# Kernel optimization log

Measured on AMD Instinct MI355X. Metric: run time of the kernel, lower is better.

## Reference

```python
import jax, jax.numpy as jnp
import numpy as np

N_NODES = 100000
N_EDGES = 1600000
EMBED = 64
HEADS = 8
HEAD_DIM = EMBED // HEADS
FFN = 4 * EMBED
EPS = 1e-5


def _layer_norm(x, g, b):
    m = jnp.mean(x, axis=-1, keepdims=True)
    v = jnp.mean(jnp.square(x - m), axis=-1, keepdims=True)
    return (x - m) * jax.lax.rsqrt(v + EPS) * g + b


def setup_inputs() -> dict:
    key = jax.random.key(0)
    ks = jax.random.split(key, 10)
    s = lambda fan_in: 1.0 / np.sqrt(fan_in)
    x = jax.random.normal(ks[0], (N_NODES, EMBED), dtype=jnp.float32)
    edge_indices = jax.random.randint(ks[1], (2, N_EDGES), 0, N_NODES, dtype=jnp.int64)
    attn_w = jax.random.uniform(ks[2], (EMBED, 3 * EMBED), jnp.float32, -s(EMBED), s(EMBED))
    attn_b = jnp.zeros((3 * EMBED,), jnp.float32)
    w1 = jax.random.uniform(ks[3], (EMBED, FFN), jnp.float32, -s(EMBED), s(EMBED))
    b1 = jnp.zeros((FFN,), jnp.float32)
    w2 = jax.random.uniform(ks[4], (FFN, EMBED), jnp.float32, -s(FFN), s(FFN))
    b2 = jnp.zeros((EMBED,), jnp.float32)
    ln1_g = jnp.ones((EMBED,), jnp.float32)
    ln1_b = jnp.zeros((EMBED,), jnp.float32)
    ln2_g = jnp.ones((EMBED,), jnp.float32)
    ln2_b = jnp.zeros((EMBED,), jnp.float32)
    return {"x": x, "edge_indices": edge_indices, "attn_w": attn_w, "attn_b": attn_b,
            "w1": w1, "b1": b1, "w2": w2, "b2": b2,
            "ln1_g": ln1_g, "ln1_b": ln1_b, "ln2_g": ln2_g, "ln2_b": ln2_b}


def _self_attention(x, edge_indices, attn_w, attn_b):
    n = x.shape[0]
    row, col = edge_indices[0], edge_indices[1]
    scale = EMBED ** (-0.5)  # note: original scales by embed_dim**-0.5
    qkv = (x @ attn_w + attn_b).reshape(n, HEADS, 3 * HEAD_DIM)
    q, k, v = jnp.split(qkv, 3, axis=2)  # each [N, H, Dh]
    alpha = jnp.sum(q[row] * k[col], axis=2) * scale  # [E, H]
    # sparse per-row softmax via segment reductions
    m = jax.ops.segment_max(alpha, row, num_segments=n)  # [N, H]
    e = jnp.exp(alpha - m[row])
    denom = jax.ops.segment_sum(e, row, num_segments=n)  # [N, H]
    weights = e / denom[row]  # [E, H]
    vals = v[col] * weights[:, :, None]  # [E, H, Dh]
    out = jax.ops.segment_sum(vals, row, num_segments=n)  # [N, H, Dh]
    return out.reshape(n, EMBED)


def reference(x, edge_indices, attn_w, attn_b, w1, b1, w2, b2, ln1_g, ln1_b, ln2_g, ln2_b):
    # post-norm (norm_first=False), dropout=0
    x = _layer_norm(x + _self_attention(x, edge_indices, attn_w, attn_b), ln1_g, ln1_b)
    ffn = jax.nn.relu(x @ w1 + b1) @ w2 + b2
    x = _layer_norm(x + ffn, ln2_g, ln2_b)
    return x
```

## Files before the change

### kernel.cpp

```cpp
#include <hip/hip_runtime.h>
#include <hip/hip_bf16.h>


#define WAVE 64
constexpr int BUCKET_SHIFT = 7;
constexpr int NBMAX = 800;

typedef __attribute__((ext_vector_type(8))) short bf16x8;
typedef __attribute__((ext_vector_type(4))) float f32x4;
typedef __attribute__((ext_vector_type(2))) float f32x2;
typedef __attribute__((ext_vector_type(2))) _Float16 h16x2;

__device__ __forceinline__ float bfbits_lo(unsigned u) {
  return __uint_as_float(u << 16);
}
__device__ __forceinline__ float bfbits_hi(unsigned u) {
  return __uint_as_float(u & 0xffff0000u);
}
__device__ __forceinline__ unsigned f2bf_pk(float a, float b) {
  unsigned ua = __float_as_uint(a);
  unsigned ub = __float_as_uint(b);
  ua = (ua + 0x7fff + ((ua >> 16) & 1)) >> 16;
  ub = (ub + 0x7fff + ((ub >> 16) & 1)) & 0xffff0000u;
  return ua | ub;
}
__device__ __forceinline__ unsigned short f2bf1(float a) {
  unsigned ua = __float_as_uint(a);
  ua = (ua + 0x7fff + ((ua >> 16) & 1)) >> 16;
  return (unsigned short)ua;
}

#if defined(__has_builtin)
#if __has_builtin(__builtin_amdgcn_cvt_pkrtz)
#define HAS_PKRTZ 1
#endif
#if __has_builtin(__builtin_amdgcn_fdot2)
#define HAS_FDOT2 1
#endif
#endif

__device__ __forceinline__ unsigned f2h_pk(float a, float b) {
#ifdef HAS_PKRTZ
  auto h = __builtin_amdgcn_cvt_pkrtz(a, b);
  return __builtin_bit_cast(unsigned, h);
#else
  h16x2 h;
  h.x = (_Float16)a;
  h.y = (_Float16)b;
  return __builtin_bit_cast(unsigned, h);
#endif
}

__device__ __forceinline__ float dot8_f16(uint4 kw, uint4 qw) {
#ifdef HAS_FDOT2
  float s = __builtin_amdgcn_fdot2(__builtin_bit_cast(h16x2, kw.x),
                                   __builtin_bit_cast(h16x2, qw.x), 0.f, false);
  s = __builtin_amdgcn_fdot2(__builtin_bit_cast(h16x2, kw.y),
                             __builtin_bit_cast(h16x2, qw.y), s, false);
  s = __builtin_amdgcn_fdot2(__builtin_bit_cast(h16x2, kw.z),
                             __builtin_bit_cast(h16x2, qw.z), s, false);
  s = __builtin_amdgcn_fdot2(__builtin_bit_cast(h16x2, kw.w),
                             __builtin_bit_cast(h16x2, qw.w), s, false);
  return s;
#else
  unsigned kk[4] = {kw.x, kw.y, kw.z, kw.w};
  unsigned qq[4] = {qw.x, qw.y, qw.z, qw.w};
  float s = 0.f;
#pragma unroll
  for (int i = 0; i < 4; i++) {
    h16x2 a = __builtin_bit_cast(h16x2, kk[i]);
    h16x2 b = __builtin_bit_cast(h16x2, qq[i]);
    s += (float)a.x * (float)b.x + (float)a.y * (float)b.y;
  }
  return s;
#endif
}

__device__ __forceinline__ void acc8_f16_pk(uint4 w, h16x2 e2, h16x2 acc[4]) {
  acc[0] = __builtin_elementwise_fma(__builtin_bit_cast(h16x2, w.x), e2, acc[0]);
  acc[1] = __builtin_elementwise_fma(__builtin_bit_cast(h16x2, w.y), e2, acc[1]);
  acc[2] = __builtin_elementwise_fma(__builtin_bit_cast(h16x2, w.z), e2, acc[2]);
  acc[3] = __builtin_elementwise_fma(__builtin_bit_cast(h16x2, w.w), e2, acc[3]);
}

__global__ __launch_bounds__(256) void cvt_w2(
    const float* __restrict__ aw, const float* __restrict__ w1,
    const float* __restrict__ w2, unsigned short* __restrict__ awT,
    unsigned short* __restrict__ w1T, unsigned short* __restrict__ w2T) {
  int tid = blockIdx.x * 256 + threadIdx.x;
  int stride = gridDim.x * 256;
  for (int i = tid; i < 192 * 64; i += stride) {
    int nn = i >> 6, kk = i & 63;
    awT[i] = f2bf1(aw[kk * 192 + nn]);
  }
  for (int i = tid; i < 256 * 64; i += stride) {
    int nn = i >> 6, kk = i & 63;
    w1T[i] = f2bf1(w1[kk * 256 + nn]);
  }
  for (int i = tid; i < 64 * 256; i += stride) {
    int nn = i >> 8, kk = i & 255;
    w2T[i] = f2bf1(w2[kk * 64 + nn]);
  }
}

template <int NCOLS, int K, int MODE>
__global__ __launch_bounds__(256) void mfma_gemm(
    const unsigned short* __restrict__ A, const float* __restrict__ Af,
    const unsigned short* __restrict__ BT, const float* __restrict__ bias,
    unsigned short* __restrict__ out_q, unsigned char* __restrict__ out_kv,
    unsigned short* __restrict__ out_h,
    const unsigned short* __restrict__ resid, const float* __restrict__ g,
    const float* __restrict__ beta, float* __restrict__ out_f, int n) {
  constexpr int KP = K + 8;
  constexpr int NT = NCOLS / 16;
  constexpr int NKC = K / 32;
  __shared__ unsigned short sB[NCOLS * KP];

  const int tid = threadIdx.x;
  {
    const uint4* src = (const uint4*)BT;
    for (int idx = tid; idx < NCOLS * K / 8; idx += 256) {
      int nn = idx / (K / 8), kq = idx % (K / 8);
      *(uint4*)&sB[nn * KP + kq * 8] = src[idx];
    }
  }
  __syncthreads();

  const int wid = tid >> 6, lane = tid & 63;
  const int l15 = lane & 15, quad = lane >> 4;
  const int rowbase = blockIdx.x * 128 + wid * 32;

  bf16x8 afrag[2][NKC];
#pragma unroll
  for (int rg = 0; rg < 2; rg++) {
    int row = rowbase + rg * 16 + l15;
    if (row >= n) row = n - 1;
    if constexpr (MODE == 0) {
      const float4* ap = (const float4*)(Af + (size_t)row * K);
#pragma unroll
      for (int kc = 0; kc < NKC; kc++) {
        float4 a = ap[kc * 8 + quad * 2], b = ap[kc * 8 + quad * 2 + 1];
        union {
          unsigned u[4];
          bf16x8 v;
        } z;
        z.u[0] = f2bf_pk(a.x, a.y);
        z.u[1] = f2bf_pk(a.z, a.w);
        z.u[2] = f2bf_pk(b.x, b.y);
        z.u[3] = f2bf_pk(b.z, b.w);
        afrag[rg][kc] = z.v;
      }
    } else {
      const bf16x8* ap = (const bf16x8*)(A + (size_t)row * K);
#pragma unroll
      for (int kc = 0; kc < NKC; kc++) afrag[rg][kc] = ap[kc * 4 + quad];
    }
  }

  f32x4 acc[2][NT];
#pragma unroll
  for (int rg = 0; rg < 2; rg++)
#pragma unroll
    for (int t = 0; t < NT; t++) acc[rg][t] = (f32x4){0.f, 0.f, 0.f, 0.f};

#pragma unroll
  for (int t = 0; t < NT; t++) {
#pragma unroll
    for (int kc = 0; kc < NKC; kc++) {
      bf16x8 b = *(const bf16x8*)&sB[(t * 16 + l15) * KP + kc * 32 + quad * 8];
      acc[0][t] = __builtin_amdgcn_mfma_f32_16x16x32_bf16(b, afrag[0][kc],
                                                          acc[0][t], 0, 0, 0);
      acc[1][t] = __builtin_amdgcn_mfma_f32_16x16x32_bf16(b, afrag[1][kc],
                                                          acc[1][t], 0, 0, 0);
    }
  }

  if (MODE == 0) {
#pragma unroll
    for (int rg = 0; rg < 2; rg++) {
      int row = rowbase + rg * 16 + l15;
      if (row >= n) continue;
#pragma unroll
      for (int t = 0; t < NT; t++) {
        int c0 = t * 16 + quad * 4;
        float4 bb = *(const float4*)&bias[c0];
        float v0 = acc[rg][t].x + bb.x, v1 = acc[rg][t].y + bb.y;
        float v2 = acc[rg][t].z + bb.z, v3 = acc[rg][t].w + bb.w;
        int hh = c0 / 24, rem = c0 % 24;
        if (rem < 8) {
          v0 *= 0.125f;
          v1 *= 0.125f;
          v2 *= 0.125f;
          v3 *= 0.125f;
          *(uint2*)(out_q + (size_t)row * 64 + hh * 8 + rem) =
              make_uint2(f2h_pk(v0, v1), f2h_pk(v2, v3));
        } else if (rem < 16) {
          *(uint2*)(out_kv + ((size_t)row << 8) + hh * 16 + (rem - 8) * 2) =
              make_uint2(f2h_pk(v0, v1), f2h_pk(v2, v3));
        } else {
          *(uint2*)(out_kv + ((size_t)row << 8) + 128 + hh * 16 +
                    (rem - 16) * 2) =
              make_uint2(f2h_pk(v0, v1), f2h_pk(v2, v3));
        }
      }
    }
  } else if (MODE == 1) {
#pragma unroll
    for (int rg = 0; rg < 2; rg++) {
      int row = rowbase + rg * 16 + l15;
      if (row >= n) continue;
#pragma unroll
      for (int t = 0; t < NT; t++) {
        int c0 = t * 16 + quad * 4;
        float4 bb = *(const float4*)&bias[c0];
        float v0 = fmaxf(acc[rg][t].x + bb.x, 0.f);
        float v1 = fmaxf(acc[rg][t].y + bb.y, 0.f);
        float v2 = fmaxf(acc[rg][t].z + bb.z, 0.f);
        float v3 = fmaxf(acc[rg][t].w + bb.w, 0.f);
        *(uint2*)(out_h + (size_t)row * NCOLS + c0) =
            make_uint2(f2bf_pk(v0, v1), f2bf_pk(v2, v3));
      }
    }
  } else {
#pragma unroll
    for (int rg = 0; rg < 2; rg++) {
      int row = rowbase + rg * 16 + l15;
      bool ok = row < n;
      int rowc = ok ? row : n - 1;
      float vals[4][4];
      float ps = 0.f, pq = 0.f;
#pragma unroll
      for (int t = 0; t < 4; t++) {
        int c0 = t * 16 + quad * 4;
        float4 bb = *(const float4*)&bias[c0];
        uint2 rr = *(const uint2*)&resid[(size_t)rowc * 64 + c0];
        vals[t][0] = acc[rg][t].x + bb.x + bfbits_lo(rr.x);
        vals[t][1] = acc[rg][t].y + bb.y + bfbits_hi(rr.x);
        vals[t][2] = acc[rg][t].z + bb.z + bfbits_lo(rr.y);
        vals[t][3] = acc[rg][t].w + bb.w + bfbits_hi(rr.y);
#pragma unroll
        for (int r = 0; r < 4; r++) {
          ps += vals[t][r];
          pq += vals[t][r] * vals[t][r];
        }
      }
      ps += __shfl_xor(ps, 16);
      ps += __shfl_xor(ps, 32);
      pq += __shfl_xor(pq, 16);
      pq += __shfl_xor(pq, 32);
      float mean = ps * (1.f / 64.f);
      float var = pq * (1.f / 64.f) - mean * mean;
      float inv = rsqrtf(var + 1e-5f);
      if (ok) {
#pragma unroll
        for (int t = 0; t < 4; t++) {
          int c0 = t * 16 + quad * 4;
          float4 gg = *(const float4*)&g[c0];
          float4 be = *(const float4*)&beta[c0];
          float4 o = make_float4((vals[t][0] - mean) * inv * gg.x + be.x,
                                 (vals[t][1] - mean) * inv * gg.y + be.y,
                                 (vals[t][2] - mean) * inv * gg.z + be.z,
                                 (vals[t][3] - mean) * inv * gg.w + be.w);
          *(float4*)&out_f[(size_t)row * 64 + c0] = o;
        }
      }
    }
  }
}

__global__ void detect_kernel(const int* __restrict__ e, unsigned* flag) {
  unsigned v = 0;
  for (int i = threadIdx.x; i < 2048; i += 256) v |= (unsigned)e[2 * i + 1];
#pragma unroll
  for (int m = 1; m < WAVE; m <<= 1) v |= (unsigned)__shfl_xor((int)v, m);
  if ((threadIdx.x & 63) == 0 && v) atomicOr(flag, 1u);
}

__device__ __forceinline__ int edge_row(const int* e, int i, bool is64) {
  return is64 ? e[2 * (size_t)i] : e[i];
}
__device__ __forceinline__ int edge_col(const int* e, int i, int E, bool is64) {
  return is64 ? e[2 * ((size_t)E + i)] : e[(size_t)E + i];
}

__global__ __launch_bounds__(256) void partition_count(
    const int* __restrict__ e, int E, const unsigned* __restrict__ flag,
    int* __restrict__ G, int NB, int CH) {
  __shared__ int h[NBMAX];
  bool is64 = (*flag == 0u);
  for (int b = threadIdx.x; b < NB; b += 256) h[b] = 0;
  __syncthreads();
  int c0 = blockIdx.x * CH, c1 = min(E, c0 + CH);
  for (int i = c0 + threadIdx.x; i < c1; i += 256)
    atomicAdd(&h[edge_row(e, i, is64) >> BUCKET_SHIFT], 1);
  __syncthreads();
  for (int b = threadIdx.x; b < NB; b += 256) G[b * 256 + blockIdx.x] = h[b];
}

__global__ __launch_bounds__(1024) void scan_reduce(const int* __restrict__ in,
                                                    int n,
                                                    int* __restrict__ bsum) {
  __shared__ int sdata[16];
  int tid = threadIdx.x;
  int idx = blockIdx.x * 1024 + tid;
  int v = (idx < n) ? in[idx] : 0;
#pragma unroll
  for (int m = 1; m < WAVE; m <<= 1) v += __shfl_xor(v, m);
  if ((tid & 63) == 0) sdata[tid >> 6] = v;
  __syncthreads();
  if (tid < 16) {
    int s = sdata[tid];
#pragma unroll
    for (int m = 1; m < 16; m <<= 1) s += __shfl_xor(s, m);
    if (tid == 0) bsum[blockIdx.x] = s;
  }
}

__global__ __launch_bounds__(256) void scan_top(const int* __restrict__ bsum,
                                                int nb,
                                                int* __restrict__ bpre) {
  __shared__ int wsum[4];
  int tid = threadIdx.x;
  int lane = tid & 63, wid = tid >> 6;
  int v = (tid < nb) ? bsum[tid] : 0;
  int incl = v;
#pragma unroll
  for (int m = 1; m < WAVE; m <<= 1) {
    int t = __shfl_up(incl, m);
    if (lane >= m) incl += t;
  }
  if (lane == 63) wsum[wid] = incl;
  __syncthreads();
  int add = 0;
  for (int w = 0; w < wid; w++) add += wsum[w];
  if (tid < nb) bpre[tid] = add + incl - v;
}

__global__ __launch_bounds__(1024) void scan_apply(
    const int* __restrict__ in, int n, const int* __restrict__ bpre,
    int* __restrict__ outscan) {
  __shared__ int wtot[16];
  __shared__ int wexcl[16];
  int tid = threadIdx.x;
  int idx = blockIdx.x * 1024 + tid;
  int v = (idx < n) ? in[idx] : 0;
  int incl = v;
#pragma unroll
  for (int m = 1; m < WAVE; m <<= 1) {
    int t = __shfl_up(incl, m);
    if ((tid & 63) >= m) incl += t;
  }
  int wid = tid >> 6;
  if ((tid & 63) == 63) wtot[wid] = incl;
  __syncthreads();
  if (tid < 16) {
    int w = wtot[tid];
    int wi = w;
#pragma unroll
    for (int m = 1; m < 16; m <<= 1) {
      int t = __shfl_up(wi, m);
      if (tid >= m) wi += t;
    }
    wexcl[tid] = wi - w;
  }
  __syncthreads();
  if (idx < n) outscan[idx] = bpre[blockIdx.x] + wexcl[wid] + incl - v;
}

__global__ __launch_bounds__(256) void partition_scatter(
    const int* __restrict__ e, int E, const unsigned* __restrict__ flag,
    const int* __restrict__ scanG, unsigned* __restrict__ ebuf, int NB,
    int CH) {
  __shared__ int base[NBMAX];
  bool is64 = (*flag == 0u);
  for (int b = threadIdx.x; b < NB; b += 256)
    base[b] = scanG[b * 256 + blockIdx.x];
  __syncthreads();
  int c0 = blockIdx.x * CH, c1 = min(E, c0 + CH);
  for (int i = c0 + threadIdx.x; i < c1; i += 256) {
    int r = edge_row(e, i, is64);
    int c = edge_col(e, i, E, is64);
    int pos = atomicAdd(&base[r >> BUCKET_SHIFT], 1);
    ebuf[pos] = ((unsigned)(r & 127) << 17) | (unsigned)c;
  }
}

__global__ __launch_bounds__(256) void bucket_csr(
    const unsigned* __restrict__ ebuf, const int* __restrict__ scanG,
    int* __restrict__ ecol, int* __restrict__ rowstart, int n, int NB, int E) {
  __shared__ int cnt[128], offs[128], cur[128];
  const int b = blockIdx.x;
  const int tid = threadIdx.x;
  const int start = scanG[b * 256];
  const int end = (b + 1 < NB) ? scanG[(b + 1) * 256] : E;
  if (tid < 128) cnt[tid] = 0;
  __syncthreads();
  for (int i = start + tid; i < end; i += 256)
    atomicAdd(&cnt[(ebuf[i] >> 17) & 127], 1);
  __syncthreads();
  if (tid < 128) offs[tid] = cnt[tid];
  __syncthreads();
  for (int s = 1; s < 128; s <<= 1) {
    int t = 0;
    if (tid < 128 && tid >= s) t = offs[tid - s];
    __syncthreads();
    if (tid < 128) offs[tid] += t;
    __syncthreads();
  }
  if (tid < 128) {
    int excl = offs[tid] - cnt[tid];
    cur[tid] = start + excl;
    int gr = (b << BUCKET_SHIFT) + tid;
    if (gr < n) rowstart[gr] = start + excl;
  }
  if (b == NB - 1 && tid == 0) rowstart[n] = E;
  __syncthreads();
  for (int i = start + tid; i < end; i += 256) {
    unsigned p = ebuf[i];
    int pos = atomicAdd(&cur[(p >> 17) & 127], 1);
    ecol[pos] = (int)(p & 0x1FFFF);
  }
}

__global__ __launch_bounds__(256) void attn_ln_kernel(
    const float* __restrict__ x, const unsigned short* __restrict__ qbuf,
    const unsigned char* __restrict__ kv, const int* __restrict__ rowstart,
    const int* __restrict__ ecol, const float* __restrict__ g,
    const float* __restrict__ beta, unsigned short* __restrict__ x1b, int n) {
  int wave = threadIdx.x >> 6;
  int lane = threadIdx.x & 63;
  int node = blockIdx.x * 4 + wave;
  if (node >= n) return;
  const int e = lane >> 3, h = lane & 7;

  uint4 qp = ((const uint4*)qbuf)[(size_t)node * 8 + h];

  int start = rowstart[node];
  int cnt = rowstart[node + 1] - start;
  const int* ec = ecol + start;
  const int koff = h * 16, voff = 128 + h * 16;

  float den = 0.f;
  h16x2 acch[4];
#pragma unroll
  for (int j = 0; j < 4; j++) acch[j] = (h16x2){(_Float16)0.f, (_Float16)0.f};

  int iters = (cnt + 7) >> 3;
  int it = 0;
  for (; it + 2 <= iters; it += 2) {
    int i0 = it * 8 + e;
    int i1 = i0 + 8;
    bool v1 = i1 < cnt;
    int c0 = ec[i0];
    int c1 = ec[v1 ? i1 : i0];
    const unsigned char* r0 = kv + ((size_t)c0 << 8);
    const unsigned char* r1 = kv + ((size_t)c1 << 8);
    uint4 kw0 = *(const uint4*)(r0 + koff);
    uint4 vw0 = *(const uint4*)(r0 + voff);
    uint4 kw1 = *(const uint4*)(r1 + koff);
    uint4 vw1 = *(const uint4*)(r1 + voff);
    float a0 = dot8_f16(kw0, qp);
    float a1 = dot8_f16(kw1, qp);
    float e0 = __expf(a0);
    float e1 = v1 ? __expf(a1) : 0.f;
    den += e0 + e1;
    h16x2 ep0 = __builtin_bit_cast(h16x2, f2h_pk(e0, e0));
    h16x2 ep1 = __builtin_bit_cast(h16x2, f2h_pk(e1, e1));
    acc8_f16_pk(vw0, ep0, acch);
    acc8_f16_pk(vw1, ep1, acch);
  }
  if (it < iters) {
    int i0 = it * 8 + e;
    bool v0 = i0 < cnt;
    int c0 = ec[v0 ? i0 : 0];
    const unsigned char* r0 = kv + ((size_t)c0 << 8);
    uint4 kw0 = *(const uint4*)(r0 + koff);
    uint4 vw0 = *(const uint4*)(r0 + voff);
    float a0 = dot8_f16(kw0, qp);
    float e0 = v0 ? __expf(a0) : 0.f;
    den += e0;
    h16x2 ep0 = __builtin_bit_cast(h16x2, f2h_pk(e0, e0));
    acc8_f16_pk(vw0, ep0, acch);
  }

#pragma unroll
  for (int m = 8; m < 64; m <<= 1) {
    den += __shfl_xor(den, m);
#pragma unroll
    for (int j = 0; j < 4; j++) {
      unsigned o = __shfl_xor(__builtin_bit_cast(unsigned, acch[j]), m);
      acch[j] += __builtin_bit_cast(h16x2, o);
    }
  }

  float acc[8] = {(float)acch[0].x, (float)acch[0].y, (float)acch[1].x,
                  (float)acch[1].y, (float)acch[2].x, (float)acch[2].y,
                  (float)acch[3].x, (float)acch[3].y};

  float invden = (cnt > 0) ? 1.f / den : 0.f;

  const float* xr = x + (size_t)node * 64 + h * 8;
  float4 x0 = *(const float4*)xr;
  float4 x1 = *(const float4*)(xr + 4);
  float v[8];
  v[0] = x0.x + acc[0] * invden;
  v[1] = x0.y + acc[1] * invden;
  v[2] = x0.z + acc[2] * invden;
  v[3] = x0.w + acc[3] * invden;
  v[4] = x1.x + acc[4] * invden;
  v[5] = x1.y + acc[5] * invden;
  v[6] = x1.z + acc[6] * invden;
  v[7] = x1.w + acc[7] * invden;

  float ps = 0.f;
#pragma unroll
  for (int j = 0; j < 8; j++) ps += v[j];
#pragma unroll
  for (int m = 1; m < 8; m <<= 1) ps += __shfl_xor(ps, m);
  float mean = ps * (1.f / 64.f);
  float pq = 0.f;
#pragma unroll
  for (int j = 0; j < 8; j++) {
    float d = v[j] - mean;
    pq += d * d;
  }
#pragma unroll
  for (int m = 1; m < 8; m <<= 1) pq += __shfl_xor(pq, m);
  float inv = rsqrtf(pq * (1.f / 64.f) + 1e-5f);

  if (e == 0) {
    const float4* gr = (const float4*)(g + h * 8);
    const float4* br = (const float4*)(beta + h * 8);
    float4 ga = gr[0], gb = gr[1];
    float4 ba = br[0], bb = br[1];
    float o[8];
    o[0] = (v[0] - mean) * inv * ga.x + ba.x;
    o[1] = (v[1] - mean) * inv * ga.y + ba.y;
    o[2] = (v[2] - mean) * inv * ga.z + ba.z;
    o[3] = (v[3] - mean) * inv * ga.w + ba.w;
    o[4] = (v[4] - mean) * inv * gb.x + bb.x;
    o[5] = (v[5] - mean) * inv * gb.y + bb.y;
    o[6] = (v[6] - mean) * inv * gb.z + bb.z;
    o[7] = (v[7] - mean) * inv * gb.w + bb.w;
    *(uint4*)(x1b + (size_t)node * 64 + h * 8) =
        make_uint4(f2bf_pk(o[0], o[1]), f2bf_pk(o[2], o[3]),
                   f2bf_pk(o[4], o[5]), f2bf_pk(o[6], o[7]));
  }
}

extern "C" void kernel_launch(void* const* d_in, const int* in_sizes, int n_in,
                              void* d_out, int out_size, void* d_ws,
                              size_t ws_size, hipStream_t stream) {
  const float* x = (const float*)d_in[0];
  const int* edges = (const int*)d_in[1];
  const float* attn_w = (const float*)d_in[2];
  const float* attn_b = (const float*)d_in[3];
  const float* w1 = (const float*)d_in[4];
  const float* b1 = (const float*)d_in[5];
  const float* w2 = (const float*)d_in[6];
  const float* b2 = (const float*)d_in[7];
  const float* g1 = (const float*)d_in[8];
  const float* bb1 = (const float*)d_in[9];
  const float* g2 = (const float*)d_in[10];
  const float* bb2 = (const float*)d_in[11];

  const int N = in_sizes[0] / 64;
  const int E = in_sizes[1] / 2;
  const int NB = (N + 127) >> BUCKET_SHIFT;
  const int CH = (E + 255) / 256;
  const int NG = NB * 256;

  char* ws = (char*)d_ws;
  size_t oq = 0;
  size_t okv = oq + (size_t)N * 128;
  size_t ox1b = okv + (size_t)N * 256;
  size_t oh = ox1b + (size_t)N * 128;
  size_t oawT = oh + (size_t)N * 512;
  size_t ow1T = oawT + 192 * 64 * 2;
  size_t ow2T = ow1T + 256 * 64 * 2;
  size_t oG = ow2T + 64 * 256 * 2;
  size_t oscanG = oG + (size_t)NG * 4;
  size_t oebuf = oscanG + (size_t)NG * 4;
  size_t oecol = oebuf + (size_t)E * 4;
  size_t orowstart = oecol + (size_t)E * 4;
  size_t obsum = orowstart + (size_t)(N + 4) * 4;
  size_t obpre = obsum + 1024;
  size_t oflag = obpre + 1024;

  unsigned short* qbuf = (unsigned short*)(ws + oq);
  unsigned char* kvb = (unsigned char*)(ws + okv);
  unsigned short* x1b = (unsigned short*)(ws + ox1b);
  unsigned short* hbuf = (unsigned short*)(ws + oh);
  unsigned short* awT = (unsigned short*)(ws + oawT);
  unsigned short* w1T = (unsigned short*)(ws + ow1T);
  unsigned short* w2T = (unsigned short*)(ws + ow2T);
  int* G = (int*)(ws + oG);
  int* scanG = (int*)(ws + oscanG);
  unsigned* ebuf = (unsigned*)(ws + oebuf);
  int* ecol = (int*)(ws + oecol);
  int* rowstart = (int*)(ws + orowstart);
  int* bsum = (int*)(ws + obsum);
  int* bpre = (int*)(ws + obpre);
  unsigned* flag = (unsigned*)(ws + oflag);

  (void)hipMemsetAsync(flag, 0, 4, stream);

  cvt_w2<<<32, 256, 0, stream>>>(attn_w, w1, w2, awT, w1T, w2T);

  detect_kernel<<<1, 256, 0, stream>>>(edges, flag);
  partition_count<<<256, 256, 0, stream>>>(edges, E, flag, G, NB, CH);
  int nscan = (NG + 1023) / 1024;
  scan_reduce<<<nscan, 1024, 0, stream>>>(G, NG, bsum);
  scan_top<<<1, 256, 0, stream>>>(bsum, nscan, bpre);
  scan_apply<<<nscan, 1024, 0, stream>>>(G, NG, bpre, scanG);
  partition_scatter<<<256, 256, 0, stream>>>(edges, E, flag, scanG, ebuf, NB,
                                             CH);
  bucket_csr<<<NB, 256, 0, stream>>>(ebuf, scanG, ecol, rowstart, N, NB, E);

  const int gblocks = (N + 127) / 128;

  mfma_gemm<192, 64, 0><<<gblocks, 256, 0, stream>>>(
      nullptr, x, awT, attn_b, qbuf, kvb, nullptr, nullptr, nullptr, nullptr,
      nullptr, N);

  attn_ln_kernel<<<(N + 3) / 4, 256, 0, stream>>>(x, qbuf, kvb, rowstart, ecol,
                                                  g1, bb1, x1b, N);

  mfma_gemm<256, 64, 1><<<gblocks, 256, 0, stream>>>(
      x1b, nullptr, w1T, b1, nullptr, nullptr, hbuf, nullptr, nullptr, nullptr,
      nullptr, N);

  mfma_gemm<64, 256, 2><<<gblocks, 256, 0, stream>>>(
      hbuf, nullptr, w2T, b2, nullptr, nullptr, nullptr, x1b, g2, bb2,
      (float*)d_out, N);
}
```

Before: 288.6 us.

## Inline index-width detection, use exp2 with folded log2e, unroll attention gather by four

Drops the separate detect kernel and memset by having each partition block test the int64/int32 edge layout itself in shared memory. Folds log2(e) into the query scale so the attention kernel can use a hardware exp2. The edge loop goes from two to four in-flight gather groups, and accumulation moves from packed fp16 FMAs to fp32. This removes two launches and aims for more memory-level parallelism, but costs more ALU work and registers in the attention kernel, and every partition block now repeats the 2048-element detection read.

```diff
diff --git a/kernel.cpp b/kernel.cpp
--- a/kernel.cpp
+++ b/kernel.cpp
@@ -37,6 +37,13 @@
 #if __has_builtin(__builtin_amdgcn_fdot2)
 #define HAS_FDOT2 1
 #endif
+#if __has_builtin(__builtin_amdgcn_exp2f)
+#define EXP2F(x) __builtin_amdgcn_exp2f(x)
+#else
+#define EXP2F(x) exp2f(x)
+#endif
+#else
+#define EXP2F(x) exp2f(x)
 #endif
 
 __device__ __forceinline__ unsigned f2h_pk(float a, float b) {
@@ -76,11 +83,20 @@
 #endif
 }
 
-__device__ __forceinline__ void acc8_f16_pk(uint4 w, h16x2 e2, h16x2 acc[4]) {
-  acc[0] = __builtin_elementwise_fma(__builtin_bit_cast(h16x2, w.x), e2, acc[0]);
-  acc[1] = __builtin_elementwise_fma(__builtin_bit_cast(h16x2, w.y), e2, acc[1]);
-  acc[2] = __builtin_elementwise_fma(__builtin_bit_cast(h16x2, w.z), e2, acc[2]);
-  acc[3] = __builtin_elementwise_fma(__builtin_bit_cast(h16x2, w.w), e2, acc[3]);
+__device__ __forceinline__ void accmix8(uint4 w, float e, float acc[8]) {
+  h16x2 p;
+  p = __builtin_bit_cast(h16x2, w.x);
+  acc[0] += (float)p.x * e;
+  acc[1] += (float)p.y * e;
+  p = __builtin_bit_cast(h16x2, w.y);
+  acc[2] += (float)p.x * e;
+  acc[3] += (float)p.y * e;
+  p = __builtin_bit_cast(h16x2, w.z);
+  acc[4] += (float)p.x * e;
+  acc[5] += (float)p.y * e;
+  p = __builtin_bit_cast(h16x2, w.w);
+  acc[6] += (float)p.x * e;
+  acc[7] += (float)p.y * e;
 }
 
 __global__ __launch_bounds__(256) void cvt_w2(
@@ -176,6 +192,7 @@
   }
 
   if (MODE == 0) {
+    constexpr float QSCALE = 0.125f * 1.44269504088896f;
 #pragma unroll
     for (int rg = 0; rg < 2; rg++) {
       int row = rowbase + rg * 16 + l15;
@@ -188,10 +205,10 @@
         float v2 = acc[rg][t].z + bb.z, v3 = acc[rg][t].w + bb.w;
         int hh = c0 / 24, rem = c0 % 24;
         if (rem < 8) {
-          v0 *= 0.125f;
-          v1 *= 0.125f;
-          v2 *= 0.125f;
-          v3 *= 0.125f;
+          v0 *= QSCALE;
+          v1 *= QSCALE;
+          v2 *= QSCALE;
+          v3 *= QSCALE;
           *(uint2*)(out_q + (size_t)row * 64 + hh * 8 + rem) =
               make_uint2(f2h_pk(v0, v1), f2h_pk(v2, v3));
         } else if (rem < 16) {
@@ -268,28 +285,25 @@
   }
 }
 
-__global__ void detect_kernel(const int* __restrict__ e, unsigned* flag) {
+__device__ __forceinline__ int edge_row(const int* e, int i, bool is64) {
+  return is64 ? e[2 * (size_t)i] : e[i];
+}
+__device__ __forceinline__ int edge_col(const int* e, int i, int E, bool is64) {
+  return is64 ? e[2 * ((size_t)E + i)] : e[(size_t)E + i];
+}
+
+__global__ __launch_bounds__(256) void partition_count(
+    const int* __restrict__ e, int E, int* __restrict__ G, int NB, int CH) {
+  __shared__ int h[NBMAX];
+  __shared__ int s32;
+  if (threadIdx.x == 0) s32 = 0;
+  for (int b = threadIdx.x; b < NB; b += 256) h[b] = 0;
+  __syncthreads();
   unsigned v = 0;
   for (int i = threadIdx.x; i < 2048; i += 256) v |= (unsigned)e[2 * i + 1];
-#pragma unroll
-  for (int m = 1; m < WAVE; m <<= 1) v |= (unsigned)__shfl_xor((int)v, m);
-  if ((threadIdx.x & 63) == 0 && v) atomicOr(flag, 1u);
-}
-
-__device__ __forceinline__ int edge_row(const int* e, int i, bool is64) {
-  return is64 ? e[2 * (size_t)i] : e[i];
-}
-__device__ __forceinline__ int edge_col(const int* e, int i, int E, bool is64) {
-  return is64 ? e[2 * ((size_t)E + i)] : e[(size_t)E + i];
-}
-
-__global__ __launch_bounds__(256) void partition_count(
-    const int* __restrict__ e, int E, const unsigned* __restrict__ flag,
-    int* __restrict__ G, int NB, int CH) {
-  __shared__ int h[NBMAX];
-  bool is64 = (*flag == 0u);
-  for (int b = threadIdx.x; b < NB; b += 256) h[b] = 0;
-  __syncthreads();
+  if (v) s32 = 1;
+  __syncthreads();
+  bool is64 = (s32 == 0);
   int c0 = blockIdx.x * CH, c1 = min(E, c0 + CH);
   for (int i = c0 + threadIdx.x; i < c1; i += 256)
     atomicAdd(&h[edge_row(e, i, is64) >> BUCKET_SHIFT], 1);
@@ -368,14 +382,19 @@
 }
 
 __global__ __launch_bounds__(256) void partition_scatter(
-    const int* __restrict__ e, int E, const unsigned* __restrict__ flag,
-    const int* __restrict__ scanG, unsigned* __restrict__ ebuf, int NB,
-    int CH) {
+    const int* __restrict__ e, int E, const int* __restrict__ scanG,
+    unsigned* __restrict__ ebuf, int NB, int CH) {
   __shared__ int base[NBMAX];
-  bool is64 = (*flag == 0u);
+  __shared__ int s32;
+  if (threadIdx.x == 0) s32 = 0;
   for (int b = threadIdx.x; b < NB; b += 256)
     base[b] = scanG[b * 256 + blockIdx.x];
   __syncthreads();
+  unsigned v = 0;
+  for (int i = threadIdx.x; i < 2048; i += 256) v |= (unsigned)e[2 * i + 1];
+  if (v) s32 = 1;
+  __syncthreads();
+  bool is64 = (s32 == 0);
   int c0 = blockIdx.x * CH, c1 = min(E, c0 + CH);
   for (int i = c0 + threadIdx.x; i < c1; i += 256) {
     int r = edge_row(e, i, is64);
@@ -420,6 +439,32 @@
     int pos = atomicAdd(&cur[(p >> 17) & 127], 1);
     ecol[pos] = (int)(p & 0x1FFFF);
   }
+}
+
+struct Grp {
+  uint4 kw, vw;
+  float m;
+};
+
+__device__ __forceinline__ Grp ldgrp(const unsigned char* __restrict__ kv,
+                                     const int* __restrict__ ec, int i,
+                                     int cnt, int koff, int voff) {
+  Grp g;
+  bool b = i < cnt;
+  int c = ec[b ? i : 0];
+  const unsigned char* r = kv + ((size_t)c << 8);
+  g.kw = *(const uint4*)(r + koff);
+  g.vw = *(const uint4*)(r + voff);
+  g.m = b ? 1.f : 0.f;
+  return g;
+}
+
+__device__ __forceinline__ void dogrp(const Grp& g, uint4 qp, float& den,
+                                      float acc[8]) {
+  float a = dot8_f16(g.kw, qp);
+  float ee = EXP2F(a) * g.m;
+  den += ee;
+  accmix8(g.vw, ee, acc);
 }
 
 __global__ __launch_bounds__(256) void attn_ln_kernel(
@@ -435,73 +480,57 @@
 
   uint4 qp = ((const uint4*)qbuf)[(size_t)node * 8 + h];
 
+  const float* xr = x + (size_t)node * 64 + h * 8;
+  float4 x0 = *(const float4*)xr;
+  float4 x1 = *(const float4*)(xr + 4);
+
   int start = rowstart[node];
   int cnt = rowstart[node + 1] - start;
   const int* ec = ecol + start;
   const int koff = h * 16, voff = 128 + h * 16;
 
   float den = 0.f;
-  h16x2 acch[4];
-#pragma unroll
-  for (int j = 0; j < 4; j++) acch[j] = (h16x2){(_Float16)0.f, (_Float16)0.f};
+  float acc[8] = {0.f, 0.f, 0.f, 0.f, 0.f, 0.f, 0.f, 0.f};
 
   int iters = (cnt + 7) >> 3;
   int it = 0;
-  for (; it + 2 <= iters; it += 2) {
-    int i0 = it * 8 + e;
-    int i1 = i0 + 8;
-    bool v1 = i1 < cnt;
-    int c0 = ec[i0];
-    int c1 = ec[v1 ? i1 : i0];
-    const unsigned char* r0 = kv + ((size_t)c0 << 8);
-    const unsigned char* r1 = kv + ((size_t)c1 << 8);
-    uint4 kw0 = *(const uint4*)(r0 + koff);
-    uint4 vw0 = *(const uint4*)(r0 + voff);
-    uint4 kw1 = *(const uint4*)(r1 + koff);
-    uint4 vw1 = *(const uint4*)(r1 + voff);
-    float a0 = dot8_f16(kw0, qp);
-    float a1 = dot8_f16(kw1, qp);
-    float e0 = __expf(a0);
-    float e1 = v1 ? __expf(a1) : 0.f;
-    den += e0 + e1;
-    h16x2 ep0 = __builtin_bit_cast(h16x2, f2h_pk(e0, e0));
-    h16x2 ep1 = __builtin_bit_cast(h16x2, f2h_pk(e1, e1));
-    acc8_f16_pk(vw0, ep0, acch);
-    acc8_f16_pk(vw1, ep1, acch);
-  }
-  if (it < iters) {
-    int i0 = it * 8 + e;
-    bool v0 = i0 < cnt;
-    int c0 = ec[v0 ? i0 : 0];
-    const unsigned char* r0 = kv + ((size_t)c0 << 8);
-    uint4 kw0 = *(const uint4*)(r0 + koff);
-    uint4 vw0 = *(const uint4*)(r0 + voff);
-    float a0 = dot8_f16(kw0, qp);
-    float e0 = v0 ? __expf(a0) : 0.f;
-    den += e0;
-    h16x2 ep0 = __builtin_bit_cast(h16x2, f2h_pk(e0, e0));
-    acc8_f16_pk(vw0, ep0, acch);
+  for (; it + 4 <= iters; it += 4) {
+    Grp g0 = ldgrp(kv, ec, it * 8 + e, cnt, koff, voff);
+    Grp g1 = ldgrp(kv, ec, it * 8 + 8 + e, cnt, koff, voff);
+    Grp g2 = ldgrp(kv, ec, it * 8 + 16 + e, cnt, koff, voff);
+    Grp g3 = ldgrp(kv, ec, it * 8 + 24 + e, cnt, koff, voff);
+    dogrp(g0, qp, den, acc);
+    dogrp(g1, qp, den, acc);
+    dogrp(g2, qp, den, acc);
+    dogrp(g3, qp, den, acc);
+  }
+  int rem = iters - it;
+  if (rem == 3) {
+    Grp g0 = ldgrp(kv, ec, it * 8 + e, cnt, koff, voff);
+    Grp g1 = ldgrp(kv, ec, it * 8 + 8 + e, cnt, koff, voff);
+    Grp g2 = ldgrp(kv, ec, it * 8 + 16 + e, cnt, koff, voff);
+    dogrp(g0, qp, den, acc);
+    dogrp(g1, qp, den, acc);
+    dogrp(g2, qp, den, acc);
+  } else if (rem == 2) {
+    Grp g0 = ldgrp(kv, ec, it * 8 + e, cnt, koff, voff);
+    Grp g1 = ldgrp(kv, ec, it * 8 + 8 + e, cnt, koff, voff);
+    dogrp(g0, qp, den, acc);
+    dogrp(g1, qp, den, acc);
+  } else if (rem == 1) {
+    Grp g0 = ldgrp(kv, ec, it * 8 + e, cnt, koff, voff);
+    dogrp(g0, qp, den, acc);
   }
 
 #pragma unroll
   for (int m = 8; m < 64; m <<= 1) {
     den += __shfl_xor(den, m);
 #pragma unroll
-    for (int j = 0; j < 4; j++) {
-      unsigned o = __shfl_xor(__builtin_bit_cast(unsigned, acch[j]), m);
-      acch[j] += __builtin_bit_cast(h16x2, o);
-    }
-  }
-
-  float acc[8] = {(float)acch[0].x, (float)acch[0].y, (float)acch[1].x,
-                  (float)acch[1].y, (float)acch[2].x, (float)acch[2].y,
-                  (float)acch[3].x, (float)acch[3].y};
+    for (int j = 0; j < 8; j++) acc[j] += __shfl_xor(acc[j], m);
+  }
 
   float invden = (cnt > 0) ? 1.f / den : 0.f;
 
-  const float* xr = x + (size_t)node * 64 + h * 8;
-  float4 x0 = *(const float4*)xr;
-  float4 x1 = *(const float4*)(xr + 4);
   float v[8];
   v[0] = x0.x + acc[0] * invden;
   v[1] = x0.y + acc[1] * invden;
@@ -585,7 +614,6 @@
   size_t orowstart = oecol + (size_t)E * 4;
   size_t obsum = orowstart + (size_t)(N + 4) * 4;
   size_t obpre = obsum + 1024;
-  size_t oflag = obpre + 1024;
 
   unsigned short* qbuf = (unsigned short*)(ws + oq);
   unsigned char* kvb = (unsigned char*)(ws + okv);
@@ -601,20 +629,15 @@
   int* rowstart = (int*)(ws + orowstart);
   int* bsum = (int*)(ws + obsum);
   int* bpre = (int*)(ws + obpre);
-  unsigned* flag = (unsigned*)(ws + oflag);
-
-  (void)hipMemsetAsync(flag, 0, 4, stream);
 
   cvt_w2<<<32, 256, 0, stream>>>(attn_w, w1, w2, awT, w1T, w2T);
 
-  detect_kernel<<<1, 256, 0, stream>>>(edges, flag);
-  partition_count<<<256, 256, 0, stream>>>(edges, E, flag, G, NB, CH);
+  partition_count<<<256, 256, 0, stream>>>(edges, E, G, NB, CH);
   int nscan = (NG + 1023) / 1024;
   scan_reduce<<<nscan, 1024, 0, stream>>>(G, NG, bsum);
   scan_top<<<1, 256, 0, stream>>>(bsum, nscan, bpre);
   scan_apply<<<nscan, 1024, 0, stream>>>(G, NG, bpre, scanG);
-  partition_scatter<<<256, 256, 0, stream>>>(edges, E, flag, scanG, ebuf, NB,
-                                             CH);
+  partition_scatter<<<256, 256, 0, stream>>>(edges, E, scanG, ebuf, NB, CH);
   bucket_csr<<<NB, 256, 0, stream>>>(ebuf, scanG, ecol, rowstart, N, NB, E);
 
   const int gblocks = (N + 127) / 128;
```

Measured after the change: 289.8 us. About the same (+0.4%).
